# Optimization experiments

Hardware: AMD Instinct MI355X
Metric: run time of the kernel (lower is better)

## Reference

```python
import jax, jax.numpy as jnp
import numpy as np

N, E, F_IN, F_E, H = 50000, 800000, 128, 16, 64
NEG_SLOPE = 0.2


def _glorot(key, shape):
    fan_in, fan_out = shape[0], shape[-1]
    lim = np.sqrt(6.0 / (fan_in + fan_out))
    return jax.random.uniform(key, shape, jnp.float32, -lim, lim)


def setup_inputs() -> dict:
    key = jax.random.key(0)
    ks = jax.random.split(key, 24)
    inp = {
        "x": jax.random.normal(ks[0], (N, F_IN), jnp.float32),
        "edge_index": jax.random.randint(ks[1], (2, E), 0, N, jnp.int64),
        "edge_attr": jax.random.normal(ks[2], (E, F_E), jnp.float32),
    }
    k = 3
    for i, f_in in zip((1, 2, 3), (F_IN, H, H)):
        inp[f"W{i}"] = _glorot(ks[k], (f_in, H)); k += 1
        inp[f"as{i}"] = _glorot(ks[k], (H,)); k += 1
        inp[f"ad{i}"] = _glorot(ks[k], (H,)); k += 1
        inp[f"We{i}"] = _glorot(ks[k], (F_E, H)); k += 1
        inp[f"ae{i}"] = _glorot(ks[k], (H,)); k += 1
        inp[f"b{i}"] = jnp.zeros((H,), jnp.float32)
        k += 1
    return inp


def gat_conv(x, src, dst, ea, W, a_s, a_d, We, a_e, b):
    # x: [N, f_in]; src/dst: [E'] (self-loops already appended); ea: [E', F_E]
    n = x.shape[0]
    h = x @ W                                   # [N, H]
    alpha_src = h @ a_s                          # [N]
    alpha_dst = h @ a_d                          # [N]
    alpha_e = (ea @ We) @ a_e                    # [E']
    alpha = alpha_src[src] + alpha_dst[dst] + alpha_e
    alpha = jnp.where(alpha > 0, alpha, NEG_SLOPE * alpha)  # leaky_relu
    # segment softmax over incoming edges of each dst node
    amax = jax.ops.segment_max(alpha, dst, num_segments=n)
    ex = jnp.exp(alpha - amax[dst])
    denom = jax.ops.segment_sum(ex, dst, num_segments=n)
    coef = ex / (denom[dst] + 1e-16)             # [E']
    out = jax.ops.segment_sum(h[src] * coef[:, None], dst, num_segments=n)
    return out + b


def reference(x, edge_index, edge_attr,
              W1, as1, ad1, We1, ae1, b1,
              W2, as2, ad2, We2, ae2, b2,
              W3, as3, ad3, We3, ae3, b3):
    n = x.shape[0]
    # add self-loops (PyG GATConv default), edge_attr fill_value='mean'
    loop = jnp.arange(n, dtype=edge_index.dtype)
    src = jnp.concatenate([edge_index[0], loop])
    dst = jnp.concatenate([edge_index[1], loop])
    ea_mean = jnp.mean(edge_attr, axis=0)
    ea = jnp.concatenate([edge_attr, jnp.broadcast_to(ea_mean, (n, edge_attr.shape[1]))], axis=0)

    x1 = jax.nn.elu(gat_conv(x, src, dst, ea, W1, as1, ad1, We1, ae1, b1))
    x2 = jax.nn.elu(gat_conv(x1, src, dst, ea, W2, as2, ad2, We2, ae2, b2))
    x3 = jax.nn.elu(gat_conv(x2, src, dst, ea, W3, as3, ad3, We3, ae3, b3))
    node_embeddings = x1 + x2 + x3
    graph_embedding = jnp.mean(node_embeddings, axis=0, keepdims=True)  # batch=None path
    return node_embeddings, graph_embedding
```

## Files before the change

kernel.cpp:

```cpp
#include <hip/hip_runtime.h>
#include <hip/hip_fp16.h>
#include <math.h>

#define HD 64
#define MAXNBK 256

typedef unsigned long long u64;
typedef _Float16 f16;
typedef _Float16 f16x8 __attribute__((ext_vector_type(8)));
typedef float f32x4 __attribute__((ext_vector_type(4)));

__device__ __forceinline__ u64 pack_rec(int src, float a0, float a1, float a2) {
    return (u64)(src & 0xFFFF)
         | ((u64)__half_as_ushort(__float2half(a0)) << 16)
         | ((u64)__half_as_ushort(__float2half(a1)) << 32)
         | ((u64)__half_as_ushort(__float2half(a2)) << 48);
}

__global__ void k_init(int* bcnt, float* gacc, int NBK) {
    int i = threadIdx.x;
    if (i < NBK) bcnt[i] = 0;
    if (i < HD) gacc[i] = 0.f;
}

__global__ void k_pre(const int* __restrict__ ei, const float* __restrict__ ea,
                      const float* We1, const float* ae1,
                      const float* We2, const float* ae2,
                      const float* We3, const float* ae3,
                      int E, int FE, u64* __restrict__ recE,
                      float* __restrict__ partials) {
    extern __shared__ float lds[];
    float* sEA = lds;
    float* su = sEA + 256 * (FE + 1);
    float* colacc = su + 3 * FE;
    int t = threadIdx.x;
    int ldE = FE + 1;

    if (t < 3 * FE) {
        int l = t / FE, f = t % FE;
        const float* We = (l == 0) ? We1 : (l == 1) ? We2 : We3;
        const float* ae = (l == 0) ? ae1 : (l == 1) ? ae2 : ae3;
        float s = 0.f;
        for (int hh = 0; hh < HD; ++hh) s += We[f * HD + hh] * ae[hh];
        su[t] = s;
    }

    const float4* ea4 = (const float4*)ea;
    size_t tot4 = (size_t)E * FE / 4;
    int per_tile4 = 64 * FE;
    size_t base4 = (size_t)blockIdx.x * per_tile4;
    float4 acc = make_float4(0.f, 0.f, 0.f, 0.f);
    for (int i = t; i < per_tile4; i += 256) {
        size_t g4 = base4 + i;
        if (g4 < tot4) {
            float4 v = ea4[g4];
            acc.x += v.x; acc.y += v.y; acc.z += v.z; acc.w += v.w;
            int g = i * 4;
            int e_loc = g / FE, f = g % FE;
            float* p = &sEA[e_loc * ldE + f];
            p[0] = v.x; p[1] = v.y; p[2] = v.z; p[3] = v.w;
        }
    }
    colacc[t * 4 + 0] = acc.x; colacc[t * 4 + 1] = acc.y;
    colacc[t * 4 + 2] = acc.z; colacc[t * 4 + 3] = acc.w;
    __syncthreads();

    int e = blockIdx.x * 256 + t;
    if (e < E) {
        float a0 = 0.f, a1 = 0.f, a2 = 0.f;
        const float* row = &sEA[t * ldE];
        for (int f = 0; f < FE; ++f) {
            float v = row[f];
            a0 += v * su[f];
            a1 += v * su[FE + f];
            a2 += v * su[2 * FE + f];
        }
        int src = ei[e];
        recE[e] = pack_rec(src, a0, a1, a2);
    }
    if (t < 16) {
        int q = t >> 2, j = t & 3;
        float s = 0.f;
        for (int k = 0; k < 64; ++k) s += colacc[(q + k * 4) * 4 + j];
        partials[blockIdx.x * 16 + (q * 4 + j)] = s;
    }
}

__global__ void k_cnt(const int* __restrict__ ei, int E, int chunk, int* bcnt, int NBK) {
    __shared__ int lc[MAXNBK];
    int t = threadIdx.x;
    lc[t] = 0;
    __syncthreads();
    int lo = blockIdx.x * chunk, hi = min(E, lo + chunk);
    for (int e = lo + t; e < hi; e += 256)
        atomicAdd(&lc[ei[E + e] >> 8], 1);
    __syncthreads();
    if (t < NBK && lc[t]) atomicAdd(&bcnt[t], lc[t]);
}

__global__ void k_u2(const float* __restrict__ partials, int NB,
                     const float* We1, const float* ae1,
                     const float* We2, const float* ae2,
                     const float* We3, const float* ae3,
                     float* sE, int FE, float invE,
                     const int* __restrict__ bcnt,
                     int* bfill , int* bbase, int NBK, int E) {
    __shared__ float red[256 * 4];
    __shared__ float uu[64];
    __shared__ float mea[16];
    __shared__ int ib[256];
    int t = threadIdx.x;
    if (t < 3 * FE) {
        int l = t / FE, f = t % FE;
        const float* We = (l == 0) ? We1 : (l == 1) ? We2 : We3;
        const float* ae = (l == 0) ? ae1 : (l == 1) ? ae2 : ae3;
        float s = 0.f;
        for (int hh = 0; hh < HD; ++hh) s += We[f * HD + hh] * ae[hh];
        uu[t] = s;
    }
    const float4* p4 = (const float4*)partials;
    int tot4 = NB * 4;
    float4 acc = make_float4(0.f, 0.f, 0.f, 0.f);
    for (int i = t; i < tot4; i += 256) {
        float4 v = p4[i];
        acc.x += v.x; acc.y += v.y; acc.z += v.z; acc.w += v.w;
    }
    red[t * 4 + 0] = acc.x; red[t * 4 + 1] = acc.y;
    red[t * 4 + 2] = acc.z; red[t * 4 + 3] = acc.w;
    int v = (t < NBK) ? bcnt[t] : 0;
    ib[t] = v;
    __syncthreads();
    for (int d = 1; d < 256; d <<= 1) {
        int x = (t >= d) ? ib[t - d] : 0;
        __syncthreads();
        ib[t] += x;
        __syncthreads();
    }
    if (t < NBK) {
        int base = ib[t] - v;
        bbase[t] = base;
        bfill[t * 16] = base;
    }
    if (t == 0) bbase[NBK] = E;
    if (t < 16) {
        int q = t >> 2, j = t & 3;
        float s = 0.f;
        for (int k = 0; k < 64; ++k) s += red[(q + k * 4) * 4 + j];
        mea[q * 4 + j] = s * invE;
    }
    __syncthreads();
    if (t < 3) {
        float a = 0.f;
        for (int f = 0; f < FE; ++f) a += mea[f] * uu[t * FE + f];
        sE[t] = a;
    }
}

__global__ void k_bucket(const int* __restrict__ ei, const u64* __restrict__ recE,
                         int E, int chunk, int* bfill ,
                         u64* __restrict__ binned, unsigned char* __restrict__ bdstl,
                         int NBK) {
    __shared__ int lcnt[MAXNBK], gb[MAXNBK], lrank[MAXNBK];
    int t = threadIdx.x;
    lcnt[t] = 0;
    __syncthreads();
    int lo = blockIdx.x * chunk, hi = min(E, lo + chunk);
    for (int e = lo + t; e < hi; e += 256)
        atomicAdd(&lcnt[ei[E + e] >> 8], 1);
    __syncthreads();
    if (t < NBK) {
        lrank[t] = 0;
        gb[t] = lcnt[t] ? atomicAdd(&bfill[t * 16], lcnt[t]) : 0;
    }
    __syncthreads();
    for (int e = lo + t; e < hi; e += 256) {
        u64 r = recE[e];
        int dst = ei[E + e];
        int b = dst >> 8;
        int rank = atomicAdd(&lrank[b], 1);
        int pos = gb[b] + rank;
        binned[pos] = r;
        bdstl[pos] = (unsigned char)(dst & 255);
    }
}

__global__ void k_sort(const int* __restrict__ bbase, const u64* __restrict__ binned,
                       const unsigned char* __restrict__ bdstl,
                       const float* __restrict__ sE,
                       int* __restrict__ row_ptr,
                       u64* __restrict__ rec, int N, int E) {
    __shared__ int lcnt[256], lfill[256];
    int b = blockIdx.x, t = threadIdx.x;
    int base = bbase[b], nrec = bbase[b + 1] - base;
    lcnt[t] = 0;
    __syncthreads();
    for (int i = t; i < nrec; i += 256)
        atomicAdd(&lcnt[bdstl[base + i]], 1);
    __syncthreads();
    int v = lcnt[t];
    for (int d = 1; d < 256; d <<= 1) {
        int x = (t >= d) ? lcnt[t - d] : 0;
        __syncthreads();
        lcnt[t] += x;
        __syncthreads();
    }
    int gnode = (b << 8) + t;
    int rp = base + gnode + (lcnt[t] - v);
    if (gnode < N) {
        row_ptr[gnode] = rp;
        rec[rp] = pack_rec(gnode, sE[0], sE[1], sE[2]);
    }
    if (b == 0 && t == 0) row_ptr[N] = E + N;
    lfill[t] = rp + 1;
    __syncthreads();
    for (int i = t; i < nrec; i += 256) {
        u64 r = binned[base + i];
        int dl = bdstl[base + i];
        int p = atomicAdd(&lfill[dl], 1);
        rec[p] = r;
    }
}

__global__ void k_gemm(const void* __restrict__ xin, int in_f16,
                       const float* __restrict__ W,
                       const float* __restrict__ a_s, const float* __restrict__ a_d,
                       __half* __restrict__ h, float* __restrict__ as_n,
                       float* __restrict__ ad_n, int N, int K) {
    extern __shared__ char smem[];
    const int SK = K + 8;
    f16* xs = (f16*)smem;
    f16* wt = xs + 64 * SK;
    int t = threadIdx.x;
    int nb = blockIdx.x * 64;

    int nK4 = K >> 2;
    if (in_f16) {
        const __half* xh = (const __half*)xin;
        for (int i = t; i < 64 * nK4; i += 256) {
            int row = i / nK4, c4 = i % nK4;
            int gr = nb + row; if (gr >= N) gr = N - 1;
            u64 v = ((const u64*)(xh + (size_t)gr * K))[c4];
            *(u64*)&xs[row * SK + c4 * 4] = v;
        }
    } else {
        const float* xf = (const float*)xin;
        for (int i = t; i < 64 * nK4; i += 256) {
            int row = i / nK4, c4 = i % nK4;
            int gr = nb + row; if (gr >= N) gr = N - 1;
            float4 v = ((const float4*)(xf + (size_t)gr * K))[c4];
            f16* p = &xs[row * SK + c4 * 4];
            p[0] = (f16)v.x; p[1] = (f16)v.y; p[2] = (f16)v.z; p[3] = (f16)v.w;
        }
    }
    for (int i = t; i < K * 64; i += 256) {
        int k = i >> 6, c = i & 63;
        wt[c * SK + k] = (f16)W[i];
    }
    __syncthreads();

    int wv = t >> 6, lane = t & 63;
    int m = lane & 15, quad = lane >> 4;
    int rowA = wv * 16 + m;

    f32x4 acc[4];
#pragma unroll
    for (int ct = 0; ct < 4; ++ct) acc[ct] = (f32x4){0.f, 0.f, 0.f, 0.f};

    for (int ks = 0; ks < (K >> 5); ++ks) {
        f16x8 a = *(const f16x8*)&xs[rowA * SK + ks * 32 + quad * 8];
#pragma unroll
        for (int ct = 0; ct < 4; ++ct) {
            f16x8 bf = *(const f16x8*)&wt[(ct * 16 + m) * SK + ks * 32 + quad * 8];
            acc[ct] = __builtin_amdgcn_mfma_f32_16x16x32_f16(a, bf, acc[ct], 0, 0, 0);
        }
    }

    __syncthreads();
    f16* ht = xs;
    const int HS = 72;
#pragma unroll
    for (int ct = 0; ct < 4; ++ct)
#pragma unroll
        for (int r = 0; r < 4; ++r) {
            int rl = wv * 16 + quad * 4 + r;
            ht[rl * HS + ct * 16 + m] = (f16)acc[ct][r];
        }
    __syncthreads();

    {
        int row = t >> 2, cb = (t & 3) * 16;
        int gr = nb + row;
        if (gr < N) {
            ulonglong2 v0 = *(const ulonglong2*)&ht[row * HS + cb];
            ulonglong2 v1 = *(const ulonglong2*)&ht[row * HS + cb + 8];
            *(ulonglong2*)(h + (size_t)gr * HD + cb) = v0;
            *(ulonglong2*)(h + (size_t)gr * HD + cb + 8) = v1;
        }
    }
    float ac = a_s[lane], adc = a_d[lane];
    for (int rr = 0; rr < 16; ++rr) {
        int row = wv * 16 + rr, gr = nb + row;
        float v = (float)ht[row * HS + lane];
        float vs = v * ac, vd = v * adc;
#pragma unroll
        for (int dd = 32; dd; dd >>= 1) {
            vs += __shfl_down(vs, dd, 64);
            vd += __shfl_down(vd, dd, 64);
        }
        if (lane == 0 && gr < N) { as_n[gr] = vs; ad_n[gr] = vd; }
    }
}

__global__ void k_aggr(const __half* __restrict__ h, const float* __restrict__ as_n,
                       const float* __restrict__ ad_n, const int* __restrict__ row_ptr,
                       const u64* __restrict__ rec, int l,
                       const float* __restrict__ b, __half* __restrict__ x_out,
                       float* __restrict__ emb, int N, int first) {
    int wave = threadIdx.x >> 6, lane = threadIdx.x & 63;
    int n = blockIdx.x * 4 + wave;
    if (n >= N) return;
    int base = row_ptr[n], end = row_ptr[n + 1];
    float adv = ad_n[n];
    const int shift = 16 * (l + 1);
    float m = -INFINITY, d = 0.f, acc = 0.f;

    for (int c = base; c < end; c += 64) {
        int cnt = min(64, end - c);
        float a = -INFINITY;
        int s = 0;
        if (lane < cnt) {
            u64 r = rec[c + lane];
            s = (int)(r & 0xFFFFull);
            float aE = __half2float(__ushort_as_half((unsigned short)(r >> shift)));
            a = as_n[s] + adv + aE;
            a = (a > 0.f) ? a : 0.2f * a;
        }
        float mc = a;
#pragma unroll
        for (int dd = 32; dd; dd >>= 1) mc = fmaxf(mc, __shfl_xor(mc, dd, 64));
        float mn = fmaxf(m, mc);
        float w = (lane < cnt) ? __expf(a - mn) : 0.f;
        float dc = w;
#pragma unroll
        for (int dd = 32; dd; dd >>= 1) dc += __shfl_xor(dc, dd, 64);
        float sc = __expf(m - mn);
        d = d * sc + dc;
        acc = acc * sc;
        m = mn;
        int j = 0;
        for (; j + 7 < cnt; j += 8) {
            int sx[8]; float wx[8];
#pragma unroll
            for (int q = 0; q < 8; ++q) {
                sx[q] = __shfl(s, j + q, 64);
                wx[q] = __shfl(w, j + q, 64);
            }
            float hx[8];
#pragma unroll
            for (int q = 0; q < 8; ++q)
                hx[q] = __half2float(h[(size_t)sx[q] * HD + lane]);
#pragma unroll
            for (int q = 0; q < 8; ++q) acc += wx[q] * hx[q];
        }
        for (; j + 3 < cnt; j += 4) {
            int s0 = __shfl(s, j, 64), s1 = __shfl(s, j + 1, 64),
                s2 = __shfl(s, j + 2, 64), s3 = __shfl(s, j + 3, 64);
            float w0 = __shfl(w, j, 64), w1 = __shfl(w, j + 1, 64),
                  w2 = __shfl(w, j + 2, 64), w3 = __shfl(w, j + 3, 64);
            float h0 = __half2float(h[(size_t)s0 * HD + lane]);
            float h1 = __half2float(h[(size_t)s1 * HD + lane]);
            float h2 = __half2float(h[(size_t)s2 * HD + lane]);
            float h3 = __half2float(h[(size_t)s3 * HD + lane]);
            acc += w0 * h0; acc += w1 * h1; acc += w2 * h2; acc += w3 * h3;
        }
        for (; j < cnt; ++j) {
            int sj = __shfl(s, j, 64);
            float wj = __shfl(w, j, 64);
            acc += wj * __half2float(h[(size_t)sj * HD + lane]);
        }
    }

    float out = acc / (d + 1e-16f) + b[lane];
    float v = (out > 0.f) ? out : expm1f(out);
    x_out[(size_t)n * HD + lane] = __float2half(v);
    if (first) emb[(size_t)n * HD + lane] = v;
    else emb[(size_t)n * HD + lane] += v;
}

__global__ void k_red(const float* __restrict__ emb, float* gacc, int N) {
    __shared__ float lds[256];
    int f = threadIdx.x & 63, w = threadIdx.x >> 6;
    float s = 0.f;
    for (int n = blockIdx.x * 4 + w; n < N; n += gridDim.x * 4)
        s += emb[(size_t)n * HD + f];
    lds[threadIdx.x] = s;
    __syncthreads();
    if (w == 0) {
        float v = lds[f] + lds[64 + f] + lds[128 + f] + lds[192 + f];
        atomicAdd(&gacc[f], v);
    }
}

__global__ void k_div(const float* __restrict__ gacc, float* out, int N) {
    int f = threadIdx.x;
    if (f < HD) out[(size_t)N * HD + f] = gacc[f] / (float)N;
}

extern "C" void kernel_launch(void* const* d_in, const int* in_sizes, int n_in,
                              void* d_out, int out_size, void* d_ws, size_t ws_size,
                              hipStream_t stream) {
    const float* x = (const float*)d_in[0];
    const int* ei = (const int*)d_in[1];
    const float* ea = (const float*)d_in[2];

    const int FIN = in_sizes[3] / HD;
    const int N = in_sizes[0] / FIN;
    const int E = in_sizes[1] / 2;
    const int FE = in_sizes[2] / E;
    const int NBK = (N + 255) >> 8;
    const int NPRE = 512;

    const float* W[3];  const float* as_[3]; const float* ad_[3];
    const float* We[3]; const float* ae_[3]; const float* bb[3];
    for (int l = 0; l < 3; ++l) {
        W[l]  = (const float*)d_in[3 + 6 * l + 0];
        as_[l] = (const float*)d_in[3 + 6 * l + 1];
        ad_[l] = (const float*)d_in[3 + 6 * l + 2];
        We[l] = (const float*)d_in[3 + 6 * l + 3];
        ae_[l] = (const float*)d_in[3 + 6 * l + 4];
        bb[l] = (const float*)d_in[3 + 6 * l + 5];
    }

    int ntiles = (E + 255) / 256;
    int chunk = (E + NPRE - 1) / NPRE;

    char* ws = (char*)d_ws;
    size_t off = 0;
    auto alloc = [&](size_t bytes) {
        void* p = ws + off;
        off += (bytes + 255) & ~(size_t)255;
        return p;
    };
    __half* h      = (__half*)alloc((size_t)N * HD * 2);
    __half* x_cur  = (__half*)alloc((size_t)N * HD * 2);
    float*  as_n   = (float*)alloc((size_t)N * 4);
    float*  ad_n   = (float*)alloc((size_t)N * 4);
    int*    rowp   = (int*)alloc((size_t)(N + 1) * 4);
    int*    bcnt   = (int*)alloc((size_t)MAXNBK * 4);
    int*    bfill  = (int*)alloc((size_t)MAXNBK * 16 * 4);
    int*    bbase  = (int*)alloc((size_t)(MAXNBK + 1) * 4);
    u64*    rec    = (u64*)alloc((size_t)(E + N) * 8);
    u64*    recE   = (u64*)alloc((size_t)E * 8);
    u64*    binned = (u64*)alloc((size_t)E * 8);
    unsigned char* bdstl = (unsigned char*)alloc((size_t)E);
    float*  partials = (float*)alloc((size_t)ntiles * 16 * 4);
    float*  sE     = (float*)alloc(3 * 4);
    float*  gacc   = (float*)alloc(HD * 4);
    (void)ws_size; (void)n_in; (void)out_size;

    float* emb = (float*)d_out;

    k_init<<<1, 256, 0, stream>>>(bcnt, gacc, NBK);
    size_t pre_lds = (size_t)(256 * (FE + 1) + 3 * FE + 256 * 4) * 4;
    k_pre<<<ntiles, 256, pre_lds, stream>>>(ei, ea, We[0], ae_[0], We[1], ae_[1],
                                            We[2], ae_[2], E, FE, recE, partials);
    k_cnt<<<NPRE, 256, 0, stream>>>(ei, E, chunk, bcnt, NBK);
    k_u2<<<1, 256, 0, stream>>>(partials, ntiles, We[0], ae_[0], We[1], ae_[1],
                                We[2], ae_[2], sE, FE, 1.0f / (float)E,
                                bcnt, bfill, bbase, NBK, E);
    k_bucket<<<NPRE, 256, 0, stream>>>(ei, recE, E, chunk, bfill, binned, bdstl, NBK);
    k_sort<<<NBK, 256, 0, stream>>>(bbase, binned, bdstl, sE, rowp, rec, N, E);

    for (int l = 0; l < 3; ++l) {
        const void* xin = (l == 0) ? (const void*)x : (const void*)x_cur;
        int in_f16 = (l == 0) ? 0 : 1;
        int K = (l == 0) ? FIN : HD;
        size_t ldsz = (size_t)(2 * 64 * (K + 8)) * 2;
        k_gemm<<<(N + 63) / 64, 256, ldsz, stream>>>(xin, in_f16, W[l], as_[l], ad_[l],
                                                     h, as_n, ad_n, N, K);
        k_aggr<<<(N + 3) / 4, 256, 0, stream>>>(h, as_n, ad_n, rowp, rec, l,
                                                bb[l], x_cur, emb, N, (l == 0) ? 1 : 0);
    }

    k_red<<<256, 256, 0, stream>>>(emb, gacc, N);
    k_div<<<1, 64, 0, stream>>>(gacc, emb, N);
}
```

Before: 396.6 us.

## Fuse preprocessing launches, shrink buckets, vectorize aggregation gathers, fold attention dots into GEMM

Several changes at once. The We·ae projection moves into k_init. The edge-count pass is folded into k_pre as extra blocks, and k_div is merged into k_red through a last-block ticket, which removes launches. Buckets shrink from 256 to 128 nodes, giving more k_sort blocks. The aggregation kernel now has each lane gather 4 features as one 8-byte load, handling 4 edges per iteration, with a cross-quarter shuffle reduction at the end. The per-node attention dot products are computed from the MFMA accumulators in registers instead of re-reading the f16 tile. The risks are extra shuffle reductions and the correctness of the ticket-based fence logic.

```diff
diff --git a/kernel.cpp b/kernel.cpp
--- a/kernel.cpp
+++ b/kernel.cpp
@@ -3,7 +3,7 @@
 #include <math.h>
 
 #define HD 64
-#define MAXNBK 256
+#define MAXNBK 512
 
 typedef unsigned long long u64;
 typedef _Float16 f16;
@@ -17,33 +17,52 @@
          | ((u64)__half_as_ushort(__float2half(a2)) << 48);
 }
 
-__global__ void k_init(int* bcnt, float* gacc, int NBK) {
-    int i = threadIdx.x;
-    if (i < NBK) bcnt[i] = 0;
-    if (i < HD) gacc[i] = 0.f;
-}
-
-__global__ void k_pre(const int* __restrict__ ei, const float* __restrict__ ea,
-                      const float* We1, const float* ae1,
-                      const float* We2, const float* ae2,
-                      const float* We3, const float* ae3,
-                      int E, int FE, u64* __restrict__ recE,
-                      float* __restrict__ partials) {
-    extern __shared__ float lds[];
-    float* sEA = lds;
-    float* su = sEA + 256 * (FE + 1);
-    float* colacc = su + 3 * FE;
+__global__ void k_init(int* bcnt, float* gacc, int* tick, float* suG,
+                       const float* We1, const float* ae1,
+                       const float* We2, const float* ae2,
+                       const float* We3, const float* ae3, int FE) {
     int t = threadIdx.x;
-    int ldE = FE + 1;
-
+    for (int i = t; i < MAXNBK; i += 256) bcnt[i] = 0;
+    if (t < HD) gacc[t] = 0.f;
+    if (t == 0) *tick = 0;
     if (t < 3 * FE) {
         int l = t / FE, f = t % FE;
         const float* We = (l == 0) ? We1 : (l == 1) ? We2 : We3;
         const float* ae = (l == 0) ? ae1 : (l == 1) ? ae2 : ae3;
         float s = 0.f;
         for (int hh = 0; hh < HD; ++hh) s += We[f * HD + hh] * ae[hh];
-        su[t] = s;
-    }
+        suG[t] = s;
+    }
+}
+
+__global__ void k_pre(const int* __restrict__ ei, const float* __restrict__ ea,
+                      const float* __restrict__ suG,
+                      int E, int FE, u64* __restrict__ recE,
+                      float* __restrict__ partials,
+                      int ntiles, int chunk, int* bcnt, int NBK) {
+    extern __shared__ float lds[];
+    int t = threadIdx.x;
+
+    if (blockIdx.x >= ntiles) {
+        int* lc = (int*)lds;
+        for (int i = t; i < NBK; i += 256) lc[i] = 0;
+        __syncthreads();
+        int cb = blockIdx.x - ntiles;
+        int lo = cb * chunk, hi = min(E, lo + chunk);
+        for (int e = lo + t; e < hi; e += 256)
+            atomicAdd(&lc[ei[E + e] >> 7], 1);
+        __syncthreads();
+        for (int i = t; i < NBK; i += 256)
+            if (lc[i]) atomicAdd(&bcnt[i], lc[i]);
+        return;
+    }
+
+    float* sEA = lds;
+    float* su = sEA + 256 * (FE + 1);
+    float* colacc = su + 3 * FE;
+    int ldE = FE + 1;
+
+    if (t < 3 * FE) su[t] = suG[t];
 
     const float4* ea4 = (const float4*)ea;
     size_t tot4 = (size_t)E * FE / 4;
@@ -86,38 +105,15 @@
     }
 }
 
-__global__ void k_cnt(const int* __restrict__ ei, int E, int chunk, int* bcnt, int NBK) {
-    __shared__ int lc[MAXNBK];
-    int t = threadIdx.x;
-    lc[t] = 0;
-    __syncthreads();
-    int lo = blockIdx.x * chunk, hi = min(E, lo + chunk);
-    for (int e = lo + t; e < hi; e += 256)
-        atomicAdd(&lc[ei[E + e] >> 8], 1);
-    __syncthreads();
-    if (t < NBK && lc[t]) atomicAdd(&bcnt[t], lc[t]);
-}
-
 __global__ void k_u2(const float* __restrict__ partials, int NB,
-                     const float* We1, const float* ae1,
-                     const float* We2, const float* ae2,
-                     const float* We3, const float* ae3,
+                     const float* __restrict__ suG,
                      float* sE, int FE, float invE,
                      const int* __restrict__ bcnt,
                      int* bfill , int* bbase, int NBK, int E) {
     __shared__ float red[256 * 4];
-    __shared__ float uu[64];
     __shared__ float mea[16];
     __shared__ int ib[256];
     int t = threadIdx.x;
-    if (t < 3 * FE) {
-        int l = t / FE, f = t % FE;
-        const float* We = (l == 0) ? We1 : (l == 1) ? We2 : We3;
-        const float* ae = (l == 0) ? ae1 : (l == 1) ? ae2 : ae3;
-        float s = 0.f;
-        for (int hh = 0; hh < HD; ++hh) s += We[f * HD + hh] * ae[hh];
-        uu[t] = s;
-    }
     const float4* p4 = (const float4*)partials;
     int tot4 = NB * 4;
     float4 acc = make_float4(0.f, 0.f, 0.f, 0.f);
@@ -127,8 +123,10 @@
     }
     red[t * 4 + 0] = acc.x; red[t * 4 + 1] = acc.y;
     red[t * 4 + 2] = acc.z; red[t * 4 + 3] = acc.w;
-    int v = (t < NBK) ? bcnt[t] : 0;
-    ib[t] = v;
+    int i0 = 2 * t, i1 = 2 * t + 1;
+    int c0 = (i0 < NBK) ? bcnt[i0] : 0;
+    int c1 = (i1 < NBK) ? bcnt[i1] : 0;
+    ib[t] = c0 + c1;
     __syncthreads();
     for (int d = 1; d < 256; d <<= 1) {
         int x = (t >= d) ? ib[t - d] : 0;
@@ -136,11 +134,9 @@
         ib[t] += x;
         __syncthreads();
     }
-    if (t < NBK) {
-        int base = ib[t] - v;
-        bbase[t] = base;
-        bfill[t * 16] = base;
-    }
+    int excl = ib[t] - (c0 + c1);
+    if (i0 < NBK) { bbase[i0] = excl;      bfill[i0 * 16] = excl; }
+    if (i1 < NBK) { bbase[i1] = excl + c0; bfill[i1 * 16] = excl + c0; }
     if (t == 0) bbase[NBK] = E;
     if (t < 16) {
         int q = t >> 2, j = t & 3;
@@ -151,7 +147,7 @@
     __syncthreads();
     if (t < 3) {
         float a = 0.f;
-        for (int f = 0; f < FE; ++f) a += mea[f] * uu[t * FE + f];
+        for (int f = 0; f < FE; ++f) a += mea[f] * suG[t * FE + f];
         sE[t] = a;
     }
 }
@@ -162,25 +158,25 @@
                          int NBK) {
     __shared__ int lcnt[MAXNBK], gb[MAXNBK], lrank[MAXNBK];
     int t = threadIdx.x;
-    lcnt[t] = 0;
+    for (int i = t; i < NBK; i += 256) lcnt[i] = 0;
     __syncthreads();
     int lo = blockIdx.x * chunk, hi = min(E, lo + chunk);
     for (int e = lo + t; e < hi; e += 256)
-        atomicAdd(&lcnt[ei[E + e] >> 8], 1);
-    __syncthreads();
-    if (t < NBK) {
-        lrank[t] = 0;
-        gb[t] = lcnt[t] ? atomicAdd(&bfill[t * 16], lcnt[t]) : 0;
+        atomicAdd(&lcnt[ei[E + e] >> 7], 1);
+    __syncthreads();
+    for (int i = t; i < NBK; i += 256) {
+        lrank[i] = 0;
+        gb[i] = lcnt[i] ? atomicAdd(&bfill[i * 16], lcnt[i]) : 0;
     }
     __syncthreads();
     for (int e = lo + t; e < hi; e += 256) {
         u64 r = recE[e];
         int dst = ei[E + e];
-        int b = dst >> 8;
+        int b = dst >> 7;
         int rank = atomicAdd(&lrank[b], 1);
         int pos = gb[b] + rank;
         binned[pos] = r;
-        bdstl[pos] = (unsigned char)(dst & 255);
+        bdstl[pos] = (unsigned char)(dst & 127);
     }
 }
 
@@ -189,29 +185,31 @@
                        const float* __restrict__ sE,
                        int* __restrict__ row_ptr,
                        u64* __restrict__ rec, int N, int E) {
-    __shared__ int lcnt[256], lfill[256];
+    __shared__ int lcnt[128], lfill[128];
     int b = blockIdx.x, t = threadIdx.x;
     int base = bbase[b], nrec = bbase[b + 1] - base;
-    lcnt[t] = 0;
+    if (t < 128) lcnt[t] = 0;
     __syncthreads();
     for (int i = t; i < nrec; i += 256)
         atomicAdd(&lcnt[bdstl[base + i]], 1);
     __syncthreads();
-    int v = lcnt[t];
-    for (int d = 1; d < 256; d <<= 1) {
-        int x = (t >= d) ? lcnt[t - d] : 0;
+    int v = (t < 128) ? lcnt[t] : 0;
+    for (int d = 1; d < 128; d <<= 1) {
+        int x = (t >= d && t < 128) ? lcnt[t - d] : 0;
         __syncthreads();
-        lcnt[t] += x;
+        if (t < 128) lcnt[t] += x;
         __syncthreads();
     }
-    int gnode = (b << 8) + t;
-    int rp = base + gnode + (lcnt[t] - v);
-    if (gnode < N) {
-        row_ptr[gnode] = rp;
-        rec[rp] = pack_rec(gnode, sE[0], sE[1], sE[2]);
+    int gnode = (b << 7) + t;
+    if (t < 128) {
+        int rp = base + gnode + (lcnt[t] - v);
+        if (gnode < N) {
+            row_ptr[gnode] = rp;
+            rec[rp] = pack_rec(gnode, sE[0], sE[1], sE[2]);
+        }
+        lfill[t] = rp + 1;
     }
     if (b == 0 && t == 0) row_ptr[N] = E + N;
-    lfill[t] = rp + 1;
     __syncthreads();
     for (int i = t; i < nrec; i += 256) {
         u64 r = binned[base + i];
@@ -275,6 +273,31 @@
         }
     }
 
+    {
+        float as_c[4], ad_c[4];
+#pragma unroll
+        for (int ct = 0; ct < 4; ++ct) {
+            as_c[ct] = a_s[ct * 16 + m];
+            ad_c[ct] = a_d[ct * 16 + m];
+        }
+#pragma unroll
+        for (int r = 0; r < 4; ++r) {
+            float ps = acc[0][r] * as_c[0] + acc[1][r] * as_c[1]
+                     + acc[2][r] * as_c[2] + acc[3][r] * as_c[3];
+            float pd = acc[0][r] * ad_c[0] + acc[1][r] * ad_c[1]
+                     + acc[2][r] * ad_c[2] + acc[3][r] * ad_c[3];
+#pragma unroll
+            for (int dd = 8; dd; dd >>= 1) {
+                ps += __shfl_xor(ps, dd, 64);
+                pd += __shfl_xor(pd, dd, 64);
+            }
+            if (m == 0) {
+                int gr = nb + wv * 16 + quad * 4 + r;
+                if (gr < N) { as_n[gr] = ps; ad_n[gr] = pd; }
+            }
+        }
+    }
+
     __syncthreads();
     f16* ht = xs;
     const int HS = 72;
@@ -296,18 +319,6 @@
             *(ulonglong2*)(h + (size_t)gr * HD + cb) = v0;
             *(ulonglong2*)(h + (size_t)gr * HD + cb + 8) = v1;
         }
-    }
-    float ac = a_s[lane], adc = a_d[lane];
-    for (int rr = 0; rr < 16; ++rr) {
-        int row = wv * 16 + rr, gr = nb + row;
-        float v = (float)ht[row * HS + lane];
-        float vs = v * ac, vd = v * adc;
-#pragma unroll
-        for (int dd = 32; dd; dd >>= 1) {
-            vs += __shfl_down(vs, dd, 64);
-            vd += __shfl_down(vd, dd, 64);
-        }
-        if (lane == 0 && gr < N) { as_n[gr] = vs; ad_n[gr] = vd; }
     }
 }
 
@@ -322,7 +333,9 @@
     int base = row_ptr[n], end = row_ptr[n + 1];
     float adv = ad_n[n];
     const int shift = 16 * (l + 1);
-    float m = -INFINITY, d = 0.f, acc = 0.f;
+    int qq = lane >> 4, fq = lane & 15;
+    float m = -INFINITY, d = 0.f;
+    f32x4 acc = {0.f, 0.f, 0.f, 0.f};
 
     for (int c = base; c < end; c += 64) {
         int cnt = min(64, end - c);
@@ -345,50 +358,54 @@
         for (int dd = 32; dd; dd >>= 1) dc += __shfl_xor(dc, dd, 64);
         float sc = __expf(m - mn);
         d = d * sc + dc;
-        acc = acc * sc;
+        acc[0] *= sc; acc[1] *= sc; acc[2] *= sc; acc[3] *= sc;
         m = mn;
-        int j = 0;
-        for (; j + 7 < cnt; j += 8) {
-            int sx[8]; float wx[8];
-#pragma unroll
-            for (int q = 0; q < 8; ++q) {
-                sx[q] = __shfl(s, j + q, 64);
-                wx[q] = __shfl(w, j + q, 64);
-            }
-            float hx[8];
-#pragma unroll
-            for (int q = 0; q < 8; ++q)
-                hx[q] = __half2float(h[(size_t)sx[q] * HD + lane]);
-#pragma unroll
-            for (int q = 0; q < 8; ++q) acc += wx[q] * hx[q];
-        }
-        for (; j + 3 < cnt; j += 4) {
-            int s0 = __shfl(s, j, 64), s1 = __shfl(s, j + 1, 64),
-                s2 = __shfl(s, j + 2, 64), s3 = __shfl(s, j + 3, 64);
-            float w0 = __shfl(w, j, 64), w1 = __shfl(w, j + 1, 64),
-                  w2 = __shfl(w, j + 2, 64), w3 = __shfl(w, j + 3, 64);
-            float h0 = __half2float(h[(size_t)s0 * HD + lane]);
-            float h1 = __half2float(h[(size_t)s1 * HD + lane]);
-            float h2 = __half2float(h[(size_t)s2 * HD + lane]);
-            float h3 = __half2float(h[(size_t)s3 * HD + lane]);
-            acc += w0 * h0; acc += w1 * h1; acc += w2 * h2; acc += w3 * h3;
-        }
-        for (; j < cnt; ++j) {
+        int iters = (cnt + 3) >> 2;
+        for (int j4 = 0; j4 < iters; ++j4) {
+            int j = (j4 << 2) + qq;
             int sj = __shfl(s, j, 64);
             float wj = __shfl(w, j, 64);
-            acc += wj * __half2float(h[(size_t)sj * HD + lane]);
-        }
-    }
-
-    float out = acc / (d + 1e-16f) + b[lane];
-    float v = (out > 0.f) ? out : expm1f(out);
-    x_out[(size_t)n * HD + lane] = __float2half(v);
-    if (first) emb[(size_t)n * HD + lane] = v;
-    else emb[(size_t)n * HD + lane] += v;
-}
-
-__global__ void k_red(const float* __restrict__ emb, float* gacc, int N) {
+            u64 hv = *(const u64*)(h + (size_t)sj * HD + (fq << 2));
+            __half2 h0 = *(__half2*)&hv;
+            __half2 h1 = *((__half2*)&hv + 1);
+            float2 f0 = __half22float2(h0);
+            float2 f1 = __half22float2(h1);
+            acc[0] += wj * f0.x; acc[1] += wj * f0.y;
+            acc[2] += wj * f1.x; acc[3] += wj * f1.y;
+        }
+    }
+
+#pragma unroll
+    for (int cc = 0; cc < 4; ++cc) {
+        acc[cc] += __shfl_xor(acc[cc], 32, 64);
+        acc[cc] += __shfl_xor(acc[cc], 16, 64);
+    }
+    float inv = 1.f / (d + 1e-16f);
+    float4 b4 = ((const float4*)b)[fq];
+    float v0 = acc[0] * inv + b4.x; v0 = (v0 > 0.f) ? v0 : expm1f(v0);
+    float v1 = acc[1] * inv + b4.y; v1 = (v1 > 0.f) ? v1 : expm1f(v1);
+    float v2 = acc[2] * inv + b4.z; v2 = (v2 > 0.f) ? v2 : expm1f(v2);
+    float v3 = acc[3] * inv + b4.w; v3 = (v3 > 0.f) ? v3 : expm1f(v3);
+    if (qq == 0) {
+        union { u64 u; __half2 h2[2]; } ou;
+        ou.h2[0] = __floats2half2_rn(v0, v1);
+        ou.h2[1] = __floats2half2_rn(v2, v3);
+        *(u64*)(x_out + (size_t)n * HD + (fq << 2)) = ou.u;
+        float4* ep = (float4*)(emb + (size_t)n * HD) + fq;
+        if (first) {
+            *ep = make_float4(v0, v1, v2, v3);
+        } else {
+            float4 e = *ep;
+            e.x += v0; e.y += v1; e.z += v2; e.w += v3;
+            *ep = e;
+        }
+    }
+}
+
+__global__ void k_red(float* __restrict__ emb, float* __restrict__ gacc,
+                      int* __restrict__ tick, int N) {
     __shared__ float lds[256];
+    __shared__ int lastf;
     int f = threadIdx.x & 63, w = threadIdx.x >> 6;
     float s = 0.f;
     for (int n = blockIdx.x * 4 + w; n < N; n += gridDim.x * 4)
@@ -399,11 +416,16 @@
         float v = lds[f] + lds[64 + f] + lds[128 + f] + lds[192 + f];
         atomicAdd(&gacc[f], v);
     }
-}
-
-__global__ void k_div(const float* __restrict__ gacc, float* out, int N) {
-    int f = threadIdx.x;
-    if (f < HD) out[(size_t)N * HD + f] = gacc[f] / (float)N;
+    __syncthreads();
+    __threadfence();
+    if (threadIdx.x == 0)
+        lastf = (atomicAdd(tick, 1) == (int)gridDim.x - 1);
+    __syncthreads();
+    if (lastf && threadIdx.x < HD) {
+        float g = __hip_atomic_load(&gacc[threadIdx.x], __ATOMIC_RELAXED,
+                                    __HIP_MEMORY_SCOPE_AGENT);
+        emb[(size_t)N * HD + threadIdx.x] = g / (float)N;
+    }
 }
 
 extern "C" void kernel_launch(void* const* d_in, const int* in_sizes, int n_in,
@@ -417,7 +439,7 @@
     const int N = in_sizes[0] / FIN;
     const int E = in_sizes[1] / 2;
     const int FE = in_sizes[2] / E;
-    const int NBK = (N + 255) >> 8;
+    const int NBK = (N + 127) >> 7;
     const int NPRE = 512;
 
     const float* W[3];  const float* as_[3]; const float* ad_[3];
@@ -456,17 +478,18 @@
     float*  partials = (float*)alloc((size_t)ntiles * 16 * 4);
     float*  sE     = (float*)alloc(3 * 4);
     float*  gacc   = (float*)alloc(HD * 4);
+    float*  suG    = (float*)alloc(3 * 16 * 4);
+    int*    tick   = (int*)alloc(4);
     (void)ws_size; (void)n_in; (void)out_size;
 
     float* emb = (float*)d_out;
 
-    k_init<<<1, 256, 0, stream>>>(bcnt, gacc, NBK);
+    k_init<<<1, 256, 0, stream>>>(bcnt, gacc, tick, suG,
+                                  We[0], ae_[0], We[1], ae_[1], We[2], ae_[2], FE);
     size_t pre_lds = (size_t)(256 * (FE + 1) + 3 * FE + 256 * 4) * 4;
-    k_pre<<<ntiles, 256, pre_lds, stream>>>(ei, ea, We[0], ae_[0], We[1], ae_[1],
-                                            We[2], ae_[2], E, FE, recE, partials);
-    k_cnt<<<NPRE, 256, 0, stream>>>(ei, E, chunk, bcnt, NBK);
-    k_u2<<<1, 256, 0, stream>>>(partials, ntiles, We[0], ae_[0], We[1], ae_[1],
-                                We[2], ae_[2], sE, FE, 1.0f / (float)E,
+    k_pre<<<ntiles + NPRE, 256, pre_lds, stream>>>(ei, ea, suG, E, FE, recE, partials,
+                                                   ntiles, chunk, bcnt, NBK);
+    k_u2<<<1, 256, 0, stream>>>(partials, ntiles, suG, sE, FE, 1.0f / (float)E,
                                 bcnt, bfill, bbase, NBK, E);
     k_bucket<<<NPRE, 256, 0, stream>>>(ei, recE, E, chunk, bfill, binned, bdstl, NBK);
     k_sort<<<NBK, 256, 0, stream>>>(bbase, binned, bdstl, sE, rowp, rec, N, E);
@@ -482,6 +505,5 @@
                                                 bb[l], x_cur, emb, N, (l == 0) ? 1 : 0);
     }
 
-    k_red<<<256, 256, 0, stream>>>(emb, gacc, N);
-    k_div<<<1, 64, 0, stream>>>(gacc, emb, N);
-}
+    k_red<<<256, 256, 0, stream>>>(emb, gacc, tick, N);
+}
```

After: 378.6 us. 4.5% less time.
